# Kernel tuning notes

Hardware: AMD Instinct MI355X
Metric: run time of the kernel (lower is better)

Reference implementation:

```python
import jax, jax.numpy as jnp
import numpy as np

K = 16  # kNN neighbors


def _knn(xb, k):
    # xb: [N, H] -> [N, k] nearest-neighbor indices (self excluded)
    sq = jnp.sum(xb * xb, axis=-1)
    d = sq[:, None] + sq[None, :] - 2.0 * (xb @ xb.T)  # squared distances [N, N]
    n = xb.shape[0]
    big = jnp.asarray(1e30, d.dtype)
    d = d + jnp.eye(n, dtype=d.dtype) * big  # mask self-loops
    _, idx = jax.lax.top_k(-d, k)
    return idx


def _edgeconv(h, W0, b0, W1, b1, k):
    # Dynamic kNN graph on current features + EdgeConv with 2-layer MLP, aggr='add'
    idx = jax.vmap(lambda xb: _knn(xb, k))(h)                 # [B, N, k]
    xj = jax.vmap(lambda xb, ib: xb[ib])(h, idx)              # [B, N, k, H] gather neighbors
    xi = jnp.broadcast_to(h[:, :, None, :], xj.shape)         # [B, N, k, H]
    m = jnp.concatenate([xi, xj - xi], axis=-1)               # [B, N, k, 2H]
    e = jax.nn.elu(m @ W0 + b0)
    e = jax.nn.elu(e @ W1 + b1)
    return jnp.sum(e, axis=2)                                 # 'add' aggregation over neighbors


def _forward(x, W_in0, b_in0, W_in1, b_in1, W_in2, b_in2,
             W_e0, b_e0, W_e1, b_e1,
             W_o0, b_o0, W_o1, b_o1, W_o2, b_o2):
    # input network (in_layers=3)
    h = jax.nn.elu(x @ W_in0 + b_in0)
    h = jax.nn.elu(h @ W_in1 + b_in1)
    h = jax.nn.elu(h @ W_in2 + b_in2)
    # agg_layers=2 blocks of dynamic-kNN EdgeConv
    for l in range(W_e0.shape[0]):
        h = _edgeconv(h, W_e0[l], b_e0[l], W_e1[l], b_e1[l], K)
    # global max pool over nodes of each graph (pool='max')
    g = jnp.max(h, axis=1)                                    # [B, H]
    # output network (out_layers=3)
    g = jax.nn.elu(g @ W_o0 + b_o0)
    g = jax.nn.elu(g @ W_o1 + b_o1)
    logits = g @ W_o2 + b_o2
    return jax.nn.log_softmax(logits, axis=1)


def setup_inputs() -> dict:
    key = jax.random.key(0)
    ks = jax.random.split(key, 8)
    B, N, F, H, C, A = 128, 512, 5, 64, 10, 2
    s = jnp.float32(0.1)

    def w(k, shape):
        return jax.random.normal(k, shape, jnp.float32) * s

    return {
        'x': jax.random.normal(ks[0], (B, N, F), jnp.float32),
        'W_in0': w(ks[1], (F, H)), 'b_in0': jnp.zeros((H,), jnp.float32),
        'W_in1': w(ks[2], (H, H)), 'b_in1': jnp.zeros((H,), jnp.float32),
        'W_in2': w(ks[3], (H, H)), 'b_in2': jnp.zeros((H,), jnp.float32),
        'W_e0': w(ks[4], (A, 2 * H, H)), 'b_e0': jnp.zeros((A, H), jnp.float32),
        'W_e1': w(ks[5], (A, H, H)), 'b_e1': jnp.zeros((A, H), jnp.float32),
        'W_o0': w(ks[6], (H, H)), 'b_o0': jnp.zeros((H,), jnp.float32),
        'W_o1': w(ks[7], (H, H)), 'b_o1': jnp.zeros((H,), jnp.float32),
        'W_o2': w(jax.random.fold_in(key, 99), (H, C)), 'b_o2': jnp.zeros((C,), jnp.float32),
    }


def reference(x, W_in0, b_in0, W_in1, b_in1, W_in2, b_in2,
              W_e0, b_e0, W_e1, b_e1,
              W_o0, b_o0, W_o1, b_o1, W_o2, b_o2):
    return _forward(x, W_in0, b_in0, W_in1, b_in1, W_in2, b_in2,
                    W_e0, b_e0, W_e1, b_e1,
                    W_o0, b_o0, W_o1, b_o1, W_o2, b_o2)
```

## Files before the change

### kernel.cpp

```cpp
#include <hip/hip_runtime.h>
#include <cmath>

typedef _Float16 f16;
typedef _Float16 f16x8 __attribute__((ext_vector_type(8)));
typedef float f32x4 __attribute__((ext_vector_type(4)));

#define B_ 128
#define N_ 512
#define H_ 64
#define K_ 16

__device__ __forceinline__ float elu_(float x) { return x > 0.f ? x : (__expf(x) - 1.f); }
__device__ __forceinline__ unsigned umin_(unsigned a, unsigned b) { return a < b ? a : b; }
__device__ __forceinline__ unsigned umax_(unsigned a, unsigned b) { return a > b ? a : b; }
__device__ __forceinline__ f32x4 mfma16(f16x8 a, f16x8 b, f32x4 c) {
    return __builtin_amdgcn_mfma_f32_16x16x32_f16(a, b, c, 0, 0, 0);
}
__device__ __forceinline__ f32x4 splat4(float v) { f32x4 r; r[0]=v; r[1]=v; r[2]=v; r[3]=v; return r; }
__device__ __forceinline__ unsigned mbcnt_(unsigned long long mask) {
    return __builtin_amdgcn_mbcnt_hi((unsigned)(mask >> 32),
           __builtin_amdgcn_mbcnt_lo((unsigned)mask, 0u));
}

__device__ __forceinline__ void wsort64x4(unsigned v[4], int lane) {
    #pragma unroll
    for (int k = 2; k <= 64; k <<= 1) {
        #pragma unroll
        for (int j = k >> 1; j >= 1; j >>= 1) {
            const bool takemin = (((lane & k) == 0) == ((lane & j) == 0));
            #pragma unroll
            for (int rr = 0; rr < 4; ++rr) {
                unsigned o = __shfl_xor(v[rr], j);
                unsigned mn = umin_(v[rr], o), mx = umax_(v[rr], o);
                v[rr] = takemin ? mn : mx;
            }
        }
    }
}

__global__ __launch_bounds__(256) void mlp_kernel(const float* __restrict__ x,
        const float* __restrict__ W0, const float* __restrict__ b0,
        const float* __restrict__ W1, const float* __restrict__ b1,
        const float* __restrict__ W2, const float* __restrict__ b2,
        const float* __restrict__ We, const float* __restrict__ be,
        f16* __restrict__ hout, float* __restrict__ sqout,
        f16* __restrict__ Pout, f16* __restrict__ Qout)
{
    __shared__ f16 tile[4][16*72];
    const int lane = threadIdx.x & 63, wid = threadIdx.x >> 6;
    const int m = lane & 15, q = lane >> 4;
    const int rowbase = blockIdx.x*64 + wid*16;
    f16* tw = tile[wid];

    f16x8 af0, af1;
    {
        const float* xp = x + (size_t)(rowbase + m)*5;
        #pragma unroll
        for (int jj = 0; jj < 8; ++jj) { int k = q*8+jj; af0[jj] = (k < 5) ? (f16)xp[k] : (f16)0.f; }
    }
    f32x4 acc[4];
    #pragma unroll
    for (int t = 0; t < 4; ++t) {
        f16x8 bf;
        #pragma unroll
        for (int jj = 0; jj < 8; ++jj) { int k = q*8+jj; bf[jj] = (k < 5) ? (f16)W0[k*64 + t*16+m] : (f16)0.f; }
        acc[t] = splat4(b0[t*16+m]);
        acc[t] = mfma16(af0, bf, acc[t]);
    }
    #pragma unroll
    for (int t = 0; t < 4; ++t)
        #pragma unroll
        for (int r = 0; r < 4; ++r)
            tw[(q*4+r)*72 + t*16+m] = (f16)elu_(acc[t][r]);
    __syncthreads();
    af0 = *(const f16x8*)(tw + m*72 + q*8);
    af1 = *(const f16x8*)(tw + m*72 + q*8 + 32);
    __syncthreads();

    #pragma unroll
    for (int t = 0; t < 4; ++t) {
        f16x8 bfa, bfb;
        #pragma unroll
        for (int jj = 0; jj < 8; ++jj) {
            bfa[jj] = (f16)W1[(q*8+jj)*64 + t*16+m];
            bfb[jj] = (f16)W1[(q*8+jj+32)*64 + t*16+m];
        }
        acc[t] = splat4(b1[t*16+m]);
        acc[t] = mfma16(af0, bfa, acc[t]);
        acc[t] = mfma16(af1, bfb, acc[t]);
    }
    #pragma unroll
    for (int t = 0; t < 4; ++t)
        #pragma unroll
        for (int r = 0; r < 4; ++r)
            tw[(q*4+r)*72 + t*16+m] = (f16)elu_(acc[t][r]);
    __syncthreads();
    af0 = *(const f16x8*)(tw + m*72 + q*8);
    af1 = *(const f16x8*)(tw + m*72 + q*8 + 32);
    __syncthreads();

    #pragma unroll
    for (int t = 0; t < 4; ++t) {
        f16x8 bfa, bfb;
        #pragma unroll
        for (int jj = 0; jj < 8; ++jj) {
            bfa[jj] = (f16)W2[(q*8+jj)*64 + t*16+m];
            bfb[jj] = (f16)W2[(q*8+jj+32)*64 + t*16+m];
        }
        acc[t] = splat4(b2[t*16+m]);
        acc[t] = mfma16(af0, bfa, acc[t]);
        acc[t] = mfma16(af1, bfb, acc[t]);
    }
    float vv[4][4];
    float s[4] = {0.f,0.f,0.f,0.f};
    #pragma unroll
    for (int t = 0; t < 4; ++t)
        #pragma unroll
        for (int r = 0; r < 4; ++r) {
            float v = elu_(acc[t][r]);
            vv[t][r] = v;
            hout[(size_t)(rowbase + q*4 + r)*64 + t*16 + m] = (f16)v;
            s[r] += v*v;
        }
    #pragma unroll
    for (int off = 1; off <= 8; off <<= 1) {
        #pragma unroll
        for (int r = 0; r < 4; ++r) s[r] += __shfl_xor(s[r], off);
    }
    if (m == 0) {
        #pragma unroll
        for (int r = 0; r < 4; ++r) sqout[rowbase + q*4 + r] = s[r];
    }
    #pragma unroll
    for (int t = 0; t < 4; ++t)
        #pragma unroll
        for (int r = 0; r < 4; ++r)
            tw[(q*4+r)*72 + t*16+m] = (f16)vv[t][r];
    __syncthreads();
    af0 = *(const f16x8*)(tw + m*72 + q*8);
    af1 = *(const f16x8*)(tw + m*72 + q*8 + 32);

    f32x4 aP[4], aQ[4];
    #pragma unroll
    for (int t = 0; t < 4; ++t) { aP[t] = splat4(be[t*16+m]); aQ[t] = splat4(0.f); }
    #pragma unroll
    for (int cc = 0; cc < 2; ++cc) {
        const f16x8 afc = cc ? af1 : af0;
        #pragma unroll
        for (int t = 0; t < 4; ++t) {
            f16x8 bp, bq;
            #pragma unroll
            for (int jj = 0; jj < 8; ++jj) {
                float wa = We[(q*8+jj+32*cc)*64 + t*16+m];
                float wb = We[(q*8+jj+32*cc+64)*64 + t*16+m];
                bq[jj] = (f16)wb; bp[jj] = (f16)(wa - wb);
            }
            aP[t] = mfma16(afc, bp, aP[t]);
            aQ[t] = mfma16(afc, bq, aQ[t]);
        }
    }
    #pragma unroll
    for (int t = 0; t < 4; ++t)
        #pragma unroll
        for (int r = 0; r < 4; ++r) {
            Pout[(size_t)(rowbase + q*4 + r)*64 + t*16 + m] = (f16)aP[t][r];
            Qout[(size_t)(rowbase + q*4 + r)*64 + t*16 + m] = (f16)aQ[t][r];
        }
}

__global__ __launch_bounds__(256) void pq_kernel(const f16* __restrict__ h,
        const float* __restrict__ We, const float* __restrict__ be,
        f16* __restrict__ Pout, f16* __restrict__ Qout)
{
    const int lane = threadIdx.x & 63, wid = threadIdx.x >> 6;
    const int m = lane & 15, q = lane >> 4;
    const int rowbase = blockIdx.x*64 + wid*16;
    const f16* Ap = h + (size_t)(rowbase + m)*64 + q*8;
    f16x8 af0 = *(const f16x8*)Ap;
    f16x8 af1 = *(const f16x8*)(Ap + 32);
    f32x4 aP[4], aQ[4];
    #pragma unroll
    for (int t = 0; t < 4; ++t) { aP[t] = splat4(be[t*16+m]); aQ[t] = splat4(0.f); }
    #pragma unroll
    for (int cc = 0; cc < 2; ++cc) {
        const f16x8 afc = cc ? af1 : af0;
        #pragma unroll
        for (int t = 0; t < 4; ++t) {
            f16x8 bp, bq;
            #pragma unroll
            for (int jj = 0; jj < 8; ++jj) {
                float wa = We[(q*8+jj+32*cc)*64 + t*16+m];
                float wb = We[(q*8+jj+32*cc+64)*64 + t*16+m];
                bq[jj] = (f16)wb; bp[jj] = (f16)(wa - wb);
            }
            aP[t] = mfma16(afc, bp, aP[t]);
            aQ[t] = mfma16(afc, bq, aQ[t]);
        }
    }
    #pragma unroll
    for (int t = 0; t < 4; ++t)
        #pragma unroll
        for (int r = 0; r < 4; ++r) {
            Pout[(size_t)(rowbase + q*4 + r)*64 + t*16 + m] = (f16)aP[t][r];
            Qout[(size_t)(rowbase + q*4 + r)*64 + t*16 + m] = (f16)aQ[t][r];
        }
}

__global__ __launch_bounds__(256, 4) void knn_kernel(const f16* __restrict__ hin,
        const float* __restrict__ sq, int* __restrict__ idxout)
{
    __shared__ unsigned keys[16*514];
    __shared__ unsigned scratch[4][4][64];
    const int lane = threadIdx.x & 63;
    const int wid  = threadIdx.x >> 6;
    const int m = lane & 15, q = lane >> 4;
    const int b  = blockIdx.x >> 5;
    const int rt = blockIdx.x & 31;
    const int rowbase = rt*16;
    const f16* hb = hin + (size_t)b*N_*H_;
    const float* sqb = sq + b*N_;

    f16x8 af0, af1;
    {
        const f16* Ap = hb + (size_t)(rowbase + m)*64 + q*8;
        af0 = *(const f16x8*)Ap;
        af1 = *(const f16x8*)(Ap + 32);
    }
    for (int ct = wid; ct < 32; ct += 4) {
        const int colbase = ct*16;
        const f16* Bp = hb + (size_t)(colbase + m)*64 + q*8;
        f16x8 bf0 = *(const f16x8*)Bp;
        f16x8 bf1 = *(const f16x8*)(Bp + 32);
        f32x4 acc = splat4(0.f);
        acc = mfma16(af0, bf0, acc);
        acc = mfma16(af1, bf1, acc);
        const float sc = sqb[colbase + m];
        #pragma unroll
        for (int r = 0; r < 4; ++r) {
            float d = fmaf(-2.f, acc[r], sc);
            unsigned u = __float_as_uint(d);
            u = ((int)u < 0) ? ~u : (u | 0x80000000u);
            unsigned key = (u & 0xFFFFFE00u) | (unsigned)(colbase + m);
            const int rowin = q*4 + r;
            if (colbase + m == rowbase + rowin) key = 0xFFFFFFFFu;
            keys[rowin*514 + colbase + m] = key;
        }
    }
    __syncthreads();

    unsigned kk[4][8];
    #pragma unroll
    for (int rr = 0; rr < 4; ++rr) {
        const int ri = wid*4 + rr;
        #pragma unroll
        for (int s2 = 0; s2 < 8; ++s2) kk[rr][s2] = keys[ri*514 + lane + 64*s2];
    }
    unsigned v[4];
    #pragma unroll
    for (int rr = 0; rr < 4; ++rr) {
        unsigned mn = kk[rr][0];
        #pragma unroll
        for (int s2 = 1; s2 < 8; ++s2) mn = umin_(mn, kk[rr][s2]);
        v[rr] = mn;
    }
    wsort64x4(v, lane);
    unsigned T[4];
    #pragma unroll
    for (int rr = 0; rr < 4; ++rr) T[rr] = __shfl(v[rr], 15);

    unsigned cnt[4];
    #pragma unroll
    for (int rr = 0; rr < 4; ++rr) {
        unsigned c = 0;
        #pragma unroll
        for (int s2 = 0; s2 < 8; ++s2) {
            const bool p = kk[rr][s2] <= T[rr];
            unsigned long long bal = __ballot(p);
            unsigned pos = c + mbcnt_(bal);
            if (p && pos < 64u) scratch[wid][rr][pos] = kk[rr][s2];
            c += (unsigned)__popcll(bal);
        }
        cnt[rr] = c;
    }
    __syncthreads();

    unsigned cval[4];
    #pragma unroll
    for (int rr = 0; rr < 4; ++rr)
        cval[rr] = (lane < (int)umin_(cnt[rr], 64u)) ? scratch[wid][rr][lane] : 0xFFFFFFFFu;
    wsort64x4(cval, lane);

    #define CE_(x,y) { unsigned lo_ = umin_(a[x],a[y]); a[y] = umax_(a[x],a[y]); a[x] = lo_; }
    #define M16_ \
        CE_(0,8) CE_(1,9) CE_(2,10) CE_(3,11) CE_(4,12) CE_(5,13) CE_(6,14) CE_(7,15) \
        CE_(0,4) CE_(1,5) CE_(2,6) CE_(3,7) CE_(8,12) CE_(9,13) CE_(10,14) CE_(11,15) \
        CE_(0,2) CE_(1,3) CE_(4,6) CE_(5,7) CE_(8,10) CE_(9,11) CE_(12,14) CE_(13,15) \
        CE_(0,1) CE_(2,3) CE_(4,5) CE_(6,7) CE_(8,9) CE_(10,11) CE_(12,13) CE_(14,15)

    #pragma unroll
    for (int rr = 0; rr < 4; ++rr) {
        const int ri = wid*4 + rr;
        int* outp = idxout + ((size_t)b*N_ + rowbase + ri)*K_;
        if (cnt[rr] <= 64u) {
            if (lane < 16) outp[lane] = (int)(cval[rr] & 511u);
        } else {
            unsigned a[16];
            #pragma unroll
            for (int s2 = 0; s2 < 8; ++s2) a[s2] = kk[rr][s2];
            CE_(0,1) CE_(2,3) CE_(4,5) CE_(6,7)
            CE_(0,2) CE_(1,3) CE_(4,6) CE_(5,7)
            CE_(1,2) CE_(5,6)
            CE_(0,4) CE_(1,5) CE_(2,6) CE_(3,7)
            CE_(2,4) CE_(3,5)
            CE_(1,2) CE_(3,4) CE_(5,6)
            #pragma unroll
            for (int j = 0; j < 8; ++j) a[8+j] = __shfl_xor(a[7-j], 1);
            M16_
            #pragma unroll
            for (int d = 2; d <= 32; d <<= 1) {
                unsigned u2[16];
                #pragma unroll
                for (int j = 0; j < 16; ++j) u2[j] = __shfl_xor(a[j], d);
                #pragma unroll
                for (int j = 0; j < 16; ++j) a[j] = umin_(a[j], u2[15-j]);
                if (d < 32) { M16_ }
            }
            if (lane == 0) {
                #pragma unroll
                for (int j = 0; j < 16; ++j) outp[j] = (int)(a[j] & 511u);
            }
        }
    }
    #undef CE_
    #undef M16_
}

__global__ __launch_bounds__(256) void edge_kernel(const f16* __restrict__ P,
        const f16* __restrict__ Q, const int* __restrict__ idx,
        const float* __restrict__ W1, const float* __restrict__ b1,
        f16* __restrict__ out, float* __restrict__ sqout)
{
    const int lane = threadIdx.x & 63;
    const int wid  = threadIdx.x >> 6;
    const int m = lane & 15, q = lane >> 4;

    f16x8 bf[2][4];
    #pragma unroll
    for (int cc = 0; cc < 2; ++cc)
        #pragma unroll
        for (int t = 0; t < 4; ++t)
            #pragma unroll
            for (int jj = 0; jj < 8; ++jj)
                bf[cc][t][jj] = (f16)W1[(q*8 + jj + 32*cc)*64 + t*16 + m];
    float bcol[4];
    #pragma unroll
    for (int t = 0; t < 4; ++t) bcol[t] = b1[t*16 + m];

    const int node0 = blockIdx.x*64 + wid*16;
    int jv[16];
    #pragma unroll
    for (int i = 0; i < 16; ++i) jv[i] = idx[(size_t)(node0 + i)*K_ + m];

    for (int i = 0; i < 16; ++i) {
        const int r0 = node0 + i;
        const int qrow = (r0 & ~(N_-1)) + jv[i];
        f16x8 af[2];
        #pragma unroll
        for (int cc = 0; cc < 2; ++cc) {
            const int c0 = q*8 + 32*cc;
            f16x8 pv = *(const f16x8*)(P + (size_t)r0*64 + c0);
            f16x8 qv = *(const f16x8*)(Q + (size_t)qrow*64 + c0);
            #pragma unroll
            for (int jj = 0; jj < 8; ++jj)
                af[cc][jj] = (f16)elu_((float)pv[jj] + (float)qv[jj]);
        }
        f32x4 acc[4];
        #pragma unroll
        for (int t = 0; t < 4; ++t) acc[t] = splat4(bcol[t]);
        #pragma unroll
        for (int cc = 0; cc < 2; ++cc)
            #pragma unroll
            for (int t = 0; t < 4; ++t) acc[t] = mfma16(af[cc], bf[cc][t], acc[t]);
        float ssum = 0.f;
        #pragma unroll
        for (int t = 0; t < 4; ++t) {
            float s = elu_(acc[t][0]) + elu_(acc[t][1]) + elu_(acc[t][2]) + elu_(acc[t][3]);
            s += __shfl_xor(s, 16);
            s += __shfl_xor(s, 32);
            if (lane < 16) out[(size_t)r0*64 + t*16 + lane] = (f16)s;
            ssum += s*s;
        }
        #pragma unroll
        for (int off = 1; off <= 8; off <<= 1) ssum += __shfl_xor(ssum, off);
        if (lane == 0) sqout[r0] = ssum;
    }
}

__global__ __launch_bounds__(256) void final_kernel(const f16* __restrict__ hin,
        const float* __restrict__ Wo0, const float* __restrict__ bo0,
        const float* __restrict__ Wo1, const float* __restrict__ bo1,
        const float* __restrict__ Wo2, const float* __restrict__ bo2,
        float* __restrict__ out)
{
    __shared__ float red[4][64];
    __shared__ float g0[64], g1[64], g2[64], lg[10];
    const int t = threadIdx.x;
    const int b = blockIdx.x;
    const int f = t & 63, grp = t >> 6;
    float mx = -3.0e38f;
    for (int n = grp; n < N_; n += 4)
        mx = fmaxf(mx, (float)hin[((size_t)b*N_ + n)*64 + f]);
    red[grp][f] = mx;
    __syncthreads();
    if (t < 64) g0[t] = fmaxf(fmaxf(red[0][t], red[1][t]), fmaxf(red[2][t], red[3][t]));
    __syncthreads();
    if (t < 64) { float a = bo0[t]; for (int c = 0; c < 64; ++c) a += g0[c]*Wo0[c*64 + t]; g1[t] = elu_(a); }
    __syncthreads();
    if (t < 64) { float a = bo1[t]; for (int c = 0; c < 64; ++c) a += g1[c]*Wo1[c*64 + t]; g2[t] = elu_(a); }
    __syncthreads();
    if (t < 10) { float a = bo2[t]; for (int c = 0; c < 64; ++c) a += g2[c]*Wo2[c*10 + t]; lg[t] = a; }
    __syncthreads();
    if (t == 0) {
        float mxl = lg[0];
        for (int i = 1; i < 10; ++i) mxl = fmaxf(mxl, lg[i]);
        float s = 0.f;
        for (int i = 0; i < 10; ++i) s += expf(lg[i] - mxl);
        const float lse = mxl + logf(s);
        for (int i = 0; i < 10; ++i) out[b*10 + i] = lg[i] - lse;
    }
}

extern "C" void kernel_launch(void* const* d_in, const int* in_sizes, int n_in,
                              void* d_out, int out_size, void* d_ws, size_t ws_size,
                              hipStream_t stream) {
    const float* x     = (const float*)d_in[0];
    const float* W_in0 = (const float*)d_in[1];
    const float* b_in0 = (const float*)d_in[2];
    const float* W_in1 = (const float*)d_in[3];
    const float* b_in1 = (const float*)d_in[4];
    const float* W_in2 = (const float*)d_in[5];
    const float* b_in2 = (const float*)d_in[6];
    const float* W_e0  = (const float*)d_in[7];
    const float* b_e0  = (const float*)d_in[8];
    const float* W_e1  = (const float*)d_in[9];
    const float* b_e1  = (const float*)d_in[10];
    const float* Wo0   = (const float*)d_in[11];
    const float* bo0   = (const float*)d_in[12];
    const float* Wo1   = (const float*)d_in[13];
    const float* bo1   = (const float*)d_in[14];
    const float* Wo2   = (const float*)d_in[15];
    const float* bo2   = (const float*)d_in[16];

    char* ws = (char*)d_ws;
    f16*   hA   = (f16*)(ws);
    f16*   hB   = (f16*)(ws + 8388608);
    f16*   Pb   = (f16*)(ws + 16777216);
    f16*   Qb   = (f16*)(ws + 25165824);
    int*   idxb = (int*)(ws + 33554432);
    float* sqb  = (float*)(ws + 37748736);

    mlp_kernel<<<1024, 256, 0, stream>>>(x, W_in0, b_in0, W_in1, b_in1, W_in2, b_in2,
                                         W_e0, b_e0, hA, sqb, Pb, Qb);
    knn_kernel<<<4096, 256, 0, stream>>>(hA, sqb, idxb);
    edge_kernel<<<1024, 256, 0, stream>>>(Pb, Qb, idxb, W_e1, b_e1, hB, sqb);
    pq_kernel<<<1024, 256, 0, stream>>>(hB, W_e0 + 8192, b_e0 + 64, Pb, Qb);
    knn_kernel<<<4096, 256, 0, stream>>>(hB, sqb, idxb);
    edge_kernel<<<1024, 256, 0, stream>>>(Pb, Qb, idxb, W_e1 + 4096, b_e1 + 64, hA, sqb);

    final_kernel<<<128, 256, 0, stream>>>(hA, Wo0, bo0, Wo1, bo1, Wo2, bo2, (float*)d_out);
}
```

Measured before the change: 342.8 us.

## Radix-select kNN thresholds, fuse PQ projection into kNN, prefetch edge gathers

Swaps the two bitonic warp sorts in the kNN kernel for bitwise radix selection built on ballot/popcount to find the 16th-smallest key. Output is then written by rank using mbcnt. The separate pq_kernel is folded into the second kNN launch through a template flag, which removes one launch and one reread of h. The edge kernel now software-pipelines its P/Q gathers by loading the next node's rows ahead of use. The risks are more registers in the kNN and edge kernels, lower occupancy, and output order now depending on key ordering within the selected set.

```diff
diff --git a/kernel.cpp b/kernel.cpp
--- a/kernel.cpp
+++ b/kernel.cpp
@@ -20,22 +20,6 @@
 __device__ __forceinline__ unsigned mbcnt_(unsigned long long mask) {
     return __builtin_amdgcn_mbcnt_hi((unsigned)(mask >> 32),
            __builtin_amdgcn_mbcnt_lo((unsigned)mask, 0u));
-}
-
-__device__ __forceinline__ void wsort64x4(unsigned v[4], int lane) {
-    #pragma unroll
-    for (int k = 2; k <= 64; k <<= 1) {
-        #pragma unroll
-        for (int j = k >> 1; j >= 1; j >>= 1) {
-            const bool takemin = (((lane & k) == 0) == ((lane & j) == 0));
-            #pragma unroll
-            for (int rr = 0; rr < 4; ++rr) {
-                unsigned o = __shfl_xor(v[rr], j);
-                unsigned mn = umin_(v[rr], o), mx = umax_(v[rr], o);
-                v[rr] = takemin ? mn : mx;
-            }
-        }
-    }
 }
 
 __global__ __launch_bounds__(256) void mlp_kernel(const float* __restrict__ x,
@@ -168,46 +152,11 @@
         }
 }
 
-__global__ __launch_bounds__(256) void pq_kernel(const f16* __restrict__ h,
+template<bool DOPQ>
+__global__ __launch_bounds__(256, 4) void knn_kernel(const f16* __restrict__ hin,
+        const float* __restrict__ sq, int* __restrict__ idxout,
         const float* __restrict__ We, const float* __restrict__ be,
         f16* __restrict__ Pout, f16* __restrict__ Qout)
-{
-    const int lane = threadIdx.x & 63, wid = threadIdx.x >> 6;
-    const int m = lane & 15, q = lane >> 4;
-    const int rowbase = blockIdx.x*64 + wid*16;
-    const f16* Ap = h + (size_t)(rowbase + m)*64 + q*8;
-    f16x8 af0 = *(const f16x8*)Ap;
-    f16x8 af1 = *(const f16x8*)(Ap + 32);
-    f32x4 aP[4], aQ[4];
-    #pragma unroll
-    for (int t = 0; t < 4; ++t) { aP[t] = splat4(be[t*16+m]); aQ[t] = splat4(0.f); }
-    #pragma unroll
-    for (int cc = 0; cc < 2; ++cc) {
-        const f16x8 afc = cc ? af1 : af0;
-        #pragma unroll
-        for (int t = 0; t < 4; ++t) {
-            f16x8 bp, bq;
-            #pragma unroll
-            for (int jj = 0; jj < 8; ++jj) {
-                float wa = We[(q*8+jj+32*cc)*64 + t*16+m];
-                float wb = We[(q*8+jj+32*cc+64)*64 + t*16+m];
-                bq[jj] = (f16)wb; bp[jj] = (f16)(wa - wb);
-            }
-            aP[t] = mfma16(afc, bp, aP[t]);
-            aQ[t] = mfma16(afc, bq, aQ[t]);
-        }
-    }
-    #pragma unroll
-    for (int t = 0; t < 4; ++t)
-        #pragma unroll
-        for (int r = 0; r < 4; ++r) {
-            Pout[(size_t)(rowbase + q*4 + r)*64 + t*16 + m] = (f16)aP[t][r];
-            Qout[(size_t)(rowbase + q*4 + r)*64 + t*16 + m] = (f16)aQ[t][r];
-        }
-}
-
-__global__ __launch_bounds__(256, 4) void knn_kernel(const f16* __restrict__ hin,
-        const float* __restrict__ sq, int* __restrict__ idxout)
 {
     __shared__ unsigned keys[16*514];
     __shared__ unsigned scratch[4][4][64];
@@ -255,6 +204,7 @@
         #pragma unroll
         for (int s2 = 0; s2 < 8; ++s2) kk[rr][s2] = keys[ri*514 + lane + 64*s2];
     }
+
     unsigned v[4];
     #pragma unroll
     for (int rr = 0; rr < 4; ++rr) {
@@ -263,10 +213,18 @@
         for (int s2 = 1; s2 < 8; ++s2) mn = umin_(mn, kk[rr][s2]);
         v[rr] = mn;
     }
-    wsort64x4(v, lane);
-    unsigned T[4];
-    #pragma unroll
-    for (int rr = 0; rr < 4; ++rr) T[rr] = __shfl(v[rr], 15);
+    unsigned T[4] = {0u,0u,0u,0u};
+    #pragma unroll
+    for (int bit = 31; bit >= 9; --bit) {
+        #pragma unroll
+        for (int rr = 0; rr < 4; ++rr) {
+            unsigned cand = T[rr] | (1u << bit);
+            int c = __popcll(__ballot(v[rr] < cand));
+            T[rr] = (c < 16) ? cand : T[rr];
+        }
+    }
+    #pragma unroll
+    for (int rr = 0; rr < 4; ++rr) T[rr] |= 511u;
 
     unsigned cnt[4];
     #pragma unroll
@@ -288,7 +246,17 @@
     #pragma unroll
     for (int rr = 0; rr < 4; ++rr)
         cval[rr] = (lane < (int)umin_(cnt[rr], 64u)) ? scratch[wid][rr][lane] : 0xFFFFFFFFu;
-    wsort64x4(cval, lane);
+
+    unsigned M2[4] = {0u,0u,0u,0u};
+    #pragma unroll
+    for (int bit = 31; bit >= 0; --bit) {
+        #pragma unroll
+        for (int rr = 0; rr < 4; ++rr) {
+            unsigned cand = M2[rr] | (1u << bit);
+            int c = __popcll(__ballot(cval[rr] < cand));
+            M2[rr] = (c < 16) ? cand : M2[rr];
+        }
+    }
 
     #define CE_(x,y) { unsigned lo_ = umin_(a[x],a[y]); a[y] = umax_(a[x],a[y]); a[x] = lo_; }
     #define M16_ \
@@ -302,7 +270,9 @@
         const int ri = wid*4 + rr;
         int* outp = idxout + ((size_t)b*N_ + rowbase + ri)*K_;
         if (cnt[rr] <= 64u) {
-            if (lane < 16) outp[lane] = (int)(cval[rr] & 511u);
+            const bool p = cval[rr] <= M2[rr];
+            unsigned rank = mbcnt_(__ballot(p));
+            if (p) outp[rank] = (int)(cval[rr] & 511u);
         } else {
             unsigned a[16];
             #pragma unroll
@@ -333,6 +303,35 @@
     }
     #undef CE_
     #undef M16_
+
+    if (DOPQ) {
+        f32x4 aP[4], aQ[4];
+        #pragma unroll
+        for (int t = 0; t < 4; ++t) { aP[t] = splat4(be[t*16+m]); aQ[t] = splat4(0.f); }
+        #pragma unroll
+        for (int cc = 0; cc < 2; ++cc) {
+            const f16x8 afc = cc ? af1 : af0;
+            #pragma unroll
+            for (int t = 0; t < 4; ++t) {
+                f16x8 bp, bq;
+                #pragma unroll
+                for (int jj = 0; jj < 8; ++jj) {
+                    float wa = We[(q*8+jj+32*cc)*64 + t*16+m];
+                    float wb = We[(q*8+jj+32*cc+64)*64 + t*16+m];
+                    bq[jj] = (f16)wb; bp[jj] = (f16)(wa - wb);
+                }
+                aP[t] = mfma16(afc, bp, aP[t]);
+                aQ[t] = mfma16(afc, bq, aQ[t]);
+            }
+        }
+        #pragma unroll
+        for (int t = 0; t < 4; ++t)
+            #pragma unroll
+            for (int r = 0; r < 4; ++r) {
+                Pout[((size_t)b*N_ + rowbase + q*4 + r)*64 + t*16 + m] = (f16)aP[t][r];
+                Qout[((size_t)b*N_ + rowbase + q*4 + r)*64 + t*16 + m] = (f16)aQ[t][r];
+            }
+    }
 }
 
 __global__ __launch_bounds__(256) void edge_kernel(const f16* __restrict__ P,
@@ -357,22 +356,36 @@
     for (int t = 0; t < 4; ++t) bcol[t] = b1[t*16 + m];
 
     const int node0 = blockIdx.x*64 + wid*16;
+    const int base  = node0 & ~(N_-1);
+    const int c0a = q*8, c0b = q*8 + 32;
     int jv[16];
     #pragma unroll
     for (int i = 0; i < 16; ++i) jv[i] = idx[(size_t)(node0 + i)*K_ + m];
 
+    f16x8 cp0, cp1, cq0, cq1, np0, np1, nq0, nq1;
+    {
+        const size_t qr = (size_t)(base + jv[0]);
+        cp0 = *(const f16x8*)(P + (size_t)node0*64 + c0a);
+        cp1 = *(const f16x8*)(P + (size_t)node0*64 + c0b);
+        cq0 = *(const f16x8*)(Q + qr*64 + c0a);
+        cq1 = *(const f16x8*)(Q + qr*64 + c0b);
+    }
+    #pragma unroll
     for (int i = 0; i < 16; ++i) {
+        if (i < 15) {
+            const size_t r1 = (size_t)(node0 + i + 1);
+            const size_t qr = (size_t)(base + jv[i+1]);
+            np0 = *(const f16x8*)(P + r1*64 + c0a);
+            np1 = *(const f16x8*)(P + r1*64 + c0b);
+            nq0 = *(const f16x8*)(Q + qr*64 + c0a);
+            nq1 = *(const f16x8*)(Q + qr*64 + c0b);
+        }
         const int r0 = node0 + i;
-        const int qrow = (r0 & ~(N_-1)) + jv[i];
         f16x8 af[2];
         #pragma unroll
-        for (int cc = 0; cc < 2; ++cc) {
-            const int c0 = q*8 + 32*cc;
-            f16x8 pv = *(const f16x8*)(P + (size_t)r0*64 + c0);
-            f16x8 qv = *(const f16x8*)(Q + (size_t)qrow*64 + c0);
-            #pragma unroll
-            for (int jj = 0; jj < 8; ++jj)
-                af[cc][jj] = (f16)elu_((float)pv[jj] + (float)qv[jj]);
+        for (int jj = 0; jj < 8; ++jj) {
+            af[0][jj] = (f16)elu_((float)cp0[jj] + (float)cq0[jj]);
+            af[1][jj] = (f16)elu_((float)cp1[jj] + (float)cq1[jj]);
         }
         f32x4 acc[4];
         #pragma unroll
@@ -393,6 +406,7 @@
         #pragma unroll
         for (int off = 1; off <= 8; off <<= 1) ssum += __shfl_xor(ssum, off);
         if (lane == 0) sqout[r0] = ssum;
+        cp0 = np0; cp1 = np1; cq0 = nq0; cq1 = nq1;
     }
 }
 
@@ -461,10 +475,9 @@
 
     mlp_kernel<<<1024, 256, 0, stream>>>(x, W_in0, b_in0, W_in1, b_in1, W_in2, b_in2,
                                          W_e0, b_e0, hA, sqb, Pb, Qb);
-    knn_kernel<<<4096, 256, 0, stream>>>(hA, sqb, idxb);
+    knn_kernel<false><<<4096, 256, 0, stream>>>(hA, sqb, idxb, nullptr, nullptr, nullptr, nullptr);
     edge_kernel<<<1024, 256, 0, stream>>>(Pb, Qb, idxb, W_e1, b_e1, hB, sqb);
-    pq_kernel<<<1024, 256, 0, stream>>>(hB, W_e0 + 8192, b_e0 + 64, Pb, Qb);
-    knn_kernel<<<4096, 256, 0, stream>>>(hB, sqb, idxb);
+    knn_kernel<true><<<4096, 256, 0, stream>>>(hB, sqb, idxb, W_e0 + 8192, b_e0 + 64, Pb, Qb);
     edge_kernel<<<1024, 256, 0, stream>>>(Pb, Qb, idxb, W_e1 + 4096, b_e1 + 64, hA, sqb);
 
     final_kernel<<<128, 256, 0, stream>>>(hA, Wo0, bo0, Wo1, bo1, Wo2, bo2, (float*)d_out);
```

Result: slower. 404.0 us (+17.9%).
